# Kernel optimization log

Measured on AMD Instinct MI355X. Metric: run time of the kernel, lower is better.

## Reference

```python
import jax, jax.numpy as jnp
import numpy as np

MAX_ITER = 10
TAU = 1.0

def setup_inputs() -> dict:
    key = jax.random.key(0)
    s = jax.random.normal(key, (8192, 8192), dtype=jnp.float32)
    return {"s": s}

def reference(s) -> jnp.ndarray:
    # pygmtools sinkhorn (log-space): scale by 1/tau, then alternate
    # row-normalization (even iters) and column-normalization (odd iters)
    # via log-softmax; finally exponentiate.
    log_s = s / TAU
    for it in range(MAX_ITER):
        axis = 1 if it % 2 == 0 else 0  # rows first, then columns
        log_s = jax.nn.log_softmax(log_s, axis=axis)
    return jnp.exp(log_s)
```

## Files before the change

### kernel.cpp

```cpp
#include <hip/hip_runtime.h>
#include <math.h>

#define N 8192
#define NF4 2048


__device__ __forceinline__ float wave_max(float m) {
#pragma unroll
  for (int off = 32; off > 0; off >>= 1) m = fmaxf(m, __shfl_xor(m, off, 64));
  return m;
}
__device__ __forceinline__ float wave_sum(float s) {
#pragma unroll
  for (int off = 32; off > 0; off >>= 1) s += __shfl_xor(s, off, 64);
  return s;
}

__device__ __forceinline__ void process_row(
    const float4 (&buf)[8], const float4 (&vv)[8], float (&acc)[32],
    float* red, int parity, int wid, int lane, int t,
    float* __restrict__ u, int row) {
  float a[32];
#pragma unroll
  for (int k = 0; k < 8; ++k) {
    a[4 * k + 0] = buf[k].x - vv[k].x;
    a[4 * k + 1] = buf[k].y - vv[k].y;
    a[4 * k + 2] = buf[k].z - vv[k].z;
    a[4 * k + 3] = buf[k].w - vv[k].w;
  }
  float m0 = a[0], m1 = a[1], m2 = a[2], m3 = a[3];
#pragma unroll
  for (int k = 1; k < 8; ++k) {
    m0 = fmaxf(m0, a[4 * k + 0]);
    m1 = fmaxf(m1, a[4 * k + 1]);
    m2 = fmaxf(m2, a[4 * k + 2]);
    m3 = fmaxf(m3, a[4 * k + 3]);
  }
  float m = wave_max(fmaxf(fmaxf(m0, m1), fmaxf(m2, m3)));
  float* rp = red + (parity << 3);
  if (lane == 0) rp[wid] = m;
  __syncthreads();
  const float bm = fmaxf(fmaxf(rp[0], rp[1]), fmaxf(rp[2], rp[3]));
  float e[32];
  float s0 = 0.f, s1 = 0.f, s2 = 0.f, s3 = 0.f;
#pragma unroll
  for (int k = 0; k < 8; ++k) {
    e[4 * k + 0] = __expf(a[4 * k + 0] - bm);
    e[4 * k + 1] = __expf(a[4 * k + 1] - bm);
    e[4 * k + 2] = __expf(a[4 * k + 2] - bm);
    e[4 * k + 3] = __expf(a[4 * k + 3] - bm);
    s0 += e[4 * k + 0];
    s1 += e[4 * k + 1];
    s2 += e[4 * k + 2];
    s3 += e[4 * k + 3];
  }
  float ssum = wave_sum((s0 + s1) + (s2 + s3));
  if (lane == 0) rp[4 + wid] = ssum;
  __syncthreads();
  const float tot = rp[4] + rp[5] + rp[6] + rp[7];
  if (t == 0) u[row] = bm + __logf(tot);
  const float inv = 1.0f / tot;
#pragma unroll
  for (int i = 0; i < 32; ++i) acc[i] = fmaf(e[i], inv, acc[i]);
}

__global__ __launch_bounds__(256) void fused_pass(
    const float* __restrict__ s, const float* __restrict__ v,
    float* __restrict__ u, float* __restrict__ pt, int R, int use_v) {
  const int t = threadIdx.x;
  const int row0 = blockIdx.x * R;
  float4 vv[8];
  if (use_v) {
    const float4* v4 = (const float4*)v;
#pragma unroll
    for (int k = 0; k < 8; ++k) vv[k] = v4[t + k * 256];
  } else {
#pragma unroll
    for (int k = 0; k < 8; ++k) vv[k] = make_float4(0.f, 0.f, 0.f, 0.f);
  }
  float acc[32];
#pragma unroll
  for (int i = 0; i < 32; ++i) acc[i] = 0.f;
  __shared__ float red[16];
  const int wid = t >> 6, lane = t & 63;

  const float4* s4 = (const float4*)s + (size_t)row0 * NF4;
  float4 bufA[8], bufB[8];
#pragma unroll
  for (int k = 0; k < 8; ++k) bufA[k] = s4[t + k * 256];

  for (int r = 0; r < R; r += 2) {
    {
      const float4* p = s4 + (size_t)(r + 1) * NF4;
#pragma unroll
      for (int k = 0; k < 8; ++k) bufB[k] = p[t + k * 256];
    }
    process_row(bufA, vv, acc, red, 0, wid, lane, t, u, row0 + r);
    if (r + 2 < R) {
      const float4* p = s4 + (size_t)(r + 2) * NF4;
#pragma unroll
      for (int k = 0; k < 8; ++k) bufA[k] = p[t + k * 256];
    }
    process_row(bufB, vv, acc, red, 1, wid, lane, t, u, row0 + r + 1);
  }

  float4* p4 = (float4*)(pt + (size_t)blockIdx.x * N);
#pragma unroll
  for (int k = 0; k < 8; ++k)
    p4[t + k * 256] =
        make_float4(acc[4 * k], acc[4 * k + 1], acc[4 * k + 2], acc[4 * k + 3]);
}

__global__ __launch_bounds__(256) void combine1(const float* __restrict__ pt,
                                                float* __restrict__ ps,
                                                int per_group) {
  const int j = blockIdx.x * 256 + threadIdx.x;
  const int g = blockIdx.y;
  const float* p = pt + (size_t)g * per_group * N + j;
  float acc = 0.f;
  for (int c = 0; c < per_group; ++c) acc += p[(size_t)c * N];
  ps[(size_t)g * N + j] = acc;
}

__global__ __launch_bounds__(256) void combine2(const float* __restrict__ ps,
                                                float* __restrict__ v,
                                                int ngroups, int add_old) {
  const int j = blockIdx.x * 256 + threadIdx.x;
  float T = 0.f;
  for (int g = 0; g < ngroups; ++g) T += ps[(size_t)g * N + j];
  const float lv = __logf(T);
  v[j] = add_old ? v[j] + lv : lv;
}

__global__ __launch_bounds__(256) void finalize_k(const float* __restrict__ s,
                                                  const float* __restrict__ u,
                                                  const float* __restrict__ v,
                                                  float* __restrict__ out) {
  const size_t idx = (size_t)blockIdx.x * 256 + threadIdx.x;
  const int row = (int)(idx >> 11);
  const int c4 = (int)(idx & 2047);
  const float4 sv = ((const float4*)s)[idx];
  const float4 vv = ((const float4*)v)[c4];
  const float ur = u[row];
  float4 o;
  o.x = __expf(sv.x - ur - vv.x);
  o.y = __expf(sv.y - ur - vv.y);
  o.z = __expf(sv.z - ur - vv.z);
  o.w = __expf(sv.w - ur - vv.w);
  ((float4*)out)[idx] = o;
}

extern "C" void kernel_launch(void* const* d_in, const int* in_sizes, int n_in,
                              void* d_out, int out_size, void* d_ws, size_t ws_size,
                              hipStream_t stream) {
  const float* s = (const float*)d_in[0];
  float* out = (float*)d_out;
  float* ws = (float*)d_ws;

  const size_t avail = ws_size / sizeof(float);
  int nstrips = 512;
  while (nstrips > 8 && (size_t)(10 + nstrips) * N > avail) nstrips >>= 1;
  const int R = N / nstrips;
  float* u = ws;
  float* v = ws + N;
  float* ps = ws + 2 * N;
  float* pt = ws + 10 * N;
  const int G = (nstrips >= 8) ? 8 : nstrips;
  const int per_group = nstrips / G;

  for (int p = 0; p < 5; ++p) {
    fused_pass<<<nstrips, 256, 0, stream>>>(s, v, u, pt, R, p > 0 ? 1 : 0);
    combine1<<<dim3(N / 256, G), 256, 0, stream>>>(pt, ps, per_group);
    combine2<<<N / 256, 256, 0, stream>>>(ps, v, G, p > 0 ? 1 : 0);
  }
  finalize_k<<<(N / 256) * NF4, 256, 0, stream>>>(s, u, v, out);
}
```

Baseline: 782.2 us.

## Software-pipeline fused row pass across four register buffers with one barrier per row

Restructures the fused row-softmax pass into a staggered three-phase pipeline (max, exp/sum, accumulate) over four in-flight row buffers. Each row now costs one block barrier instead of two, and the loads for later rows are issued earlier to hide memory latency. The v offsets move from registers into shared memory to free registers for the extra buffers, with launch bounds asking for two blocks per CU. R becomes a template parameter, which lets the loops fully specialize. The risks are higher register pressure or spills from the four 8-float4 buffers, and extra LDS reads of v on every row.

```diff
diff --git a/kernel.cpp b/kernel.cpp
--- a/kernel.cpp
+++ b/kernel.cpp
@@ -16,93 +16,124 @@
   return s;
 }
 
-__device__ __forceinline__ void process_row(
-    const float4 (&buf)[8], const float4 (&vv)[8], float (&acc)[32],
-    float* red, int parity, int wid, int lane, int t,
-    float* __restrict__ u, int row) {
-  float a[32];
-#pragma unroll
-  for (int k = 0; k < 8; ++k) {
-    a[4 * k + 0] = buf[k].x - vv[k].x;
-    a[4 * k + 1] = buf[k].y - vv[k].y;
-    a[4 * k + 2] = buf[k].z - vv[k].z;
-    a[4 * k + 3] = buf[k].w - vv[k].w;
+template <int R>
+__global__ __launch_bounds__(256, 2) void fused_pass(
+    const float* __restrict__ s, const float* __restrict__ v,
+    float* __restrict__ u, float* __restrict__ pt, int use_v) {
+  static_assert(R % 4 == 0 && R >= 8, "pipeline needs R%4==0, R>=8");
+  const int t = threadIdx.x;
+  const int wid = t >> 6, lane = t & 63;
+  const int row0 = blockIdx.x * R;
+  __shared__ float4 vsh[8][256];
+  __shared__ float red[2][2][4];
+
+  {
+    const float4* v4 = (const float4*)v;
+#pragma unroll
+    for (int k = 0; k < 8; ++k)
+      vsh[k][t] = use_v ? v4[t + k * 256] : make_float4(0.f, 0.f, 0.f, 0.f);
   }
-  float m0 = a[0], m1 = a[1], m2 = a[2], m3 = a[3];
-#pragma unroll
-  for (int k = 1; k < 8; ++k) {
-    m0 = fmaxf(m0, a[4 * k + 0]);
-    m1 = fmaxf(m1, a[4 * k + 1]);
-    m2 = fmaxf(m2, a[4 * k + 2]);
-    m3 = fmaxf(m3, a[4 * k + 3]);
+
+  float acc[32];
+#pragma unroll
+  for (int i = 0; i < 32; ++i) acc[i] = 0.f;
+
+  const float4* s4 = (const float4*)s + (size_t)row0 * NF4;
+  float4 b0[8], b1[8], b2[8], b3[8];
+  float bmP = 0.f;
+
+  auto LOAD = [&](float4(&b)[8], int r) {
+    const float4* p = s4 + (size_t)r * NF4;
+#pragma unroll
+    for (int k = 0; k < 8; ++k) b[k] = p[t + k * 256];
+  };
+  auto P1 = [&](float4(&b)[8], int r) {
+    float m0 = -INFINITY, m1 = -INFINITY, m2 = -INFINITY, m3 = -INFINITY;
+#pragma unroll
+    for (int k = 0; k < 8; ++k) {
+      const float4 vv = vsh[k][t];
+      b[k].x -= vv.x; b[k].y -= vv.y; b[k].z -= vv.z; b[k].w -= vv.w;
+      m0 = fmaxf(m0, b[k].x); m1 = fmaxf(m1, b[k].y);
+      m2 = fmaxf(m2, b[k].z); m3 = fmaxf(m3, b[k].w);
+    }
+    const float m = wave_max(fmaxf(fmaxf(m0, m1), fmaxf(m2, m3)));
+    if (lane == 0) red[r & 1][0][wid] = m;
+  };
+  auto P2 = [&](float4(&b)[8], int r) -> float {
+    const float* rm = red[r & 1][0];
+    const float bm = fmaxf(fmaxf(rm[0], rm[1]), fmaxf(rm[2], rm[3]));
+    float s0 = 0.f, s1 = 0.f, s2 = 0.f, s3 = 0.f;
+#pragma unroll
+    for (int k = 0; k < 8; ++k) {
+      b[k].x = __expf(b[k].x - bm); b[k].y = __expf(b[k].y - bm);
+      b[k].z = __expf(b[k].z - bm); b[k].w = __expf(b[k].w - bm);
+      s0 += b[k].x; s1 += b[k].y; s2 += b[k].z; s3 += b[k].w;
+    }
+    const float ss = wave_sum((s0 + s1) + (s2 + s3));
+    if (lane == 0) red[r & 1][1][wid] = ss;
+    return bm;
+  };
+  auto P3 = [&](float4(&b)[8], int r, float bm) {
+    const float* rs = red[r & 1][1];
+    const float tot = (rs[0] + rs[1]) + (rs[2] + rs[3]);
+    const float inv = 1.0f / tot;
+#pragma unroll
+    for (int k = 0; k < 8; ++k) {
+      acc[4 * k + 0] = fmaf(b[k].x, inv, acc[4 * k + 0]);
+      acc[4 * k + 1] = fmaf(b[k].y, inv, acc[4 * k + 1]);
+      acc[4 * k + 2] = fmaf(b[k].z, inv, acc[4 * k + 2]);
+      acc[4 * k + 3] = fmaf(b[k].w, inv, acc[4 * k + 3]);
+    }
+    if (t == 0) u[row0 + r] = bm + __logf(tot);
+  };
+
+  LOAD(b0, 0);
+  LOAD(b1, 1);
+  P1(b0, 0);
+  __syncthreads();
+  LOAD(b2, 2);
+  bmP = P2(b0, 0);
+  P1(b1, 1);
+  __syncthreads();
+  LOAD(b3, 3);
+  P3(b0, 0, bmP);
+  bmP = P2(b1, 1);
+  P1(b2, 2);
+  __syncthreads();
+#pragma unroll 1
+  for (int k = 2; k <= R - 6; k += 4) {
+    LOAD(b0, k + 2);
+    P3(b1, k - 1, bmP);
+    bmP = P2(b2, k);
+    P1(b3, k + 1);
+    __syncthreads();
+
+    LOAD(b1, k + 3);
+    P3(b2, k, bmP);
+    bmP = P2(b3, k + 1);
+    P1(b0, k + 2);
+    __syncthreads();
+
+    LOAD(b2, k + 4);
+    P3(b3, k + 1, bmP);
+    bmP = P2(b0, k + 2);
+    P1(b1, k + 3);
+    __syncthreads();
+
+    LOAD(b3, k + 5);
+    P3(b0, k + 2, bmP);
+    bmP = P2(b1, k + 3);
+    P1(b2, k + 4);
+    __syncthreads();
   }
-  float m = wave_max(fmaxf(fmaxf(m0, m1), fmaxf(m2, m3)));
-  float* rp = red + (parity << 3);
-  if (lane == 0) rp[wid] = m;
-  __syncthreads();
-  const float bm = fmaxf(fmaxf(rp[0], rp[1]), fmaxf(rp[2], rp[3]));
-  float e[32];
-  float s0 = 0.f, s1 = 0.f, s2 = 0.f, s3 = 0.f;
-#pragma unroll
-  for (int k = 0; k < 8; ++k) {
-    e[4 * k + 0] = __expf(a[4 * k + 0] - bm);
-    e[4 * k + 1] = __expf(a[4 * k + 1] - bm);
-    e[4 * k + 2] = __expf(a[4 * k + 2] - bm);
-    e[4 * k + 3] = __expf(a[4 * k + 3] - bm);
-    s0 += e[4 * k + 0];
-    s1 += e[4 * k + 1];
-    s2 += e[4 * k + 2];
-    s3 += e[4 * k + 3];
-  }
-  float ssum = wave_sum((s0 + s1) + (s2 + s3));
-  if (lane == 0) rp[4 + wid] = ssum;
-  __syncthreads();
-  const float tot = rp[4] + rp[5] + rp[6] + rp[7];
-  if (t == 0) u[row] = bm + __logf(tot);
-  const float inv = 1.0f / tot;
-#pragma unroll
-  for (int i = 0; i < 32; ++i) acc[i] = fmaf(e[i], inv, acc[i]);
-}
-
-__global__ __launch_bounds__(256) void fused_pass(
-    const float* __restrict__ s, const float* __restrict__ v,
-    float* __restrict__ u, float* __restrict__ pt, int R, int use_v) {
-  const int t = threadIdx.x;
-  const int row0 = blockIdx.x * R;
-  float4 vv[8];
-  if (use_v) {
-    const float4* v4 = (const float4*)v;
-#pragma unroll
-    for (int k = 0; k < 8; ++k) vv[k] = v4[t + k * 256];
-  } else {
-#pragma unroll
-    for (int k = 0; k < 8; ++k) vv[k] = make_float4(0.f, 0.f, 0.f, 0.f);
-  }
-  float acc[32];
-#pragma unroll
-  for (int i = 0; i < 32; ++i) acc[i] = 0.f;
-  __shared__ float red[16];
-  const int wid = t >> 6, lane = t & 63;
-
-  const float4* s4 = (const float4*)s + (size_t)row0 * NF4;
-  float4 bufA[8], bufB[8];
-#pragma unroll
-  for (int k = 0; k < 8; ++k) bufA[k] = s4[t + k * 256];
-
-  for (int r = 0; r < R; r += 2) {
-    {
-      const float4* p = s4 + (size_t)(r + 1) * NF4;
-#pragma unroll
-      for (int k = 0; k < 8; ++k) bufB[k] = p[t + k * 256];
-    }
-    process_row(bufA, vv, acc, red, 0, wid, lane, t, u, row0 + r);
-    if (r + 2 < R) {
-      const float4* p = s4 + (size_t)(r + 2) * NF4;
-#pragma unroll
-      for (int k = 0; k < 8; ++k) bufA[k] = p[t + k * 256];
-    }
-    process_row(bufB, vv, acc, red, 1, wid, lane, t, u, row0 + r + 1);
-  }
+  P3(b1, R - 3, bmP);
+  bmP = P2(b2, R - 2);
+  P1(b3, R - 1);
+  __syncthreads();
+  P3(b2, R - 2, bmP);
+  bmP = P2(b3, R - 1);
+  __syncthreads();
+  P3(b3, R - 1, bmP);
 
   float4* p4 = (float4*)(pt + (size_t)blockIdx.x * N);
 #pragma unroll
@@ -159,17 +190,27 @@
 
   const size_t avail = ws_size / sizeof(float);
   int nstrips = 512;
-  while (nstrips > 8 && (size_t)(10 + nstrips) * N > avail) nstrips >>= 1;
-  const int R = N / nstrips;
+  while (nstrips > 128 && (size_t)(10 + nstrips) * N > avail) nstrips >>= 1;
   float* u = ws;
   float* v = ws + N;
   float* ps = ws + 2 * N;
   float* pt = ws + 10 * N;
-  const int G = (nstrips >= 8) ? 8 : nstrips;
+  const int G = 8;
   const int per_group = nstrips / G;
 
   for (int p = 0; p < 5; ++p) {
-    fused_pass<<<nstrips, 256, 0, stream>>>(s, v, u, pt, R, p > 0 ? 1 : 0);
+    const int use_v = p > 0 ? 1 : 0;
+    switch (nstrips) {
+      case 512:
+        fused_pass<16><<<512, 256, 0, stream>>>(s, v, u, pt, use_v);
+        break;
+      case 256:
+        fused_pass<32><<<256, 256, 0, stream>>>(s, v, u, pt, use_v);
+        break;
+      default:
+        fused_pass<64><<<128, 256, 0, stream>>>(s, v, u, pt, use_v);
+        break;
+    }
     combine1<<<dim3(N / 256, G), 256, 0, stream>>>(pt, ps, per_group);
     combine2<<<N / 256, 256, 0, stream>>>(ps, v, G, p > 0 ? 1 : 0);
   }
```

Result: slower. 964.2 us (+23.3%).

## Use 512-thread blocks with triple-buffered row prefetch and templated strip size

Applied to the files above, without the earlier changes.

The fused row pass now runs 512-thread blocks, so each thread holds 4 float4 per row instead of 8, which cuts register pressure and permits 4 blocks per CU. Row loads use a three-deep register ring buffer that prefetches two rows ahead, and the rows-per-strip count becomes a template parameter so the loop fully unrolls. The max/exp work is done in place in the load buffers to save registers. The trade-off is an eight-wave block reduction per row and a minimum strip count of 128.

```diff
diff --git a/kernel.cpp b/kernel.cpp
--- a/kernel.cpp
+++ b/kernel.cpp
@@ -16,99 +16,87 @@
   return s;
 }
 
-__device__ __forceinline__ void process_row(
-    const float4 (&buf)[8], const float4 (&vv)[8], float (&acc)[32],
-    float* red, int parity, int wid, int lane, int t,
-    float* __restrict__ u, int row) {
-  float a[32];
-#pragma unroll
-  for (int k = 0; k < 8; ++k) {
-    a[4 * k + 0] = buf[k].x - vv[k].x;
-    a[4 * k + 1] = buf[k].y - vv[k].y;
-    a[4 * k + 2] = buf[k].z - vv[k].z;
-    a[4 * k + 3] = buf[k].w - vv[k].w;
-  }
-  float m0 = a[0], m1 = a[1], m2 = a[2], m3 = a[3];
-#pragma unroll
-  for (int k = 1; k < 8; ++k) {
-    m0 = fmaxf(m0, a[4 * k + 0]);
-    m1 = fmaxf(m1, a[4 * k + 1]);
-    m2 = fmaxf(m2, a[4 * k + 2]);
-    m3 = fmaxf(m3, a[4 * k + 3]);
-  }
-  float m = wave_max(fmaxf(fmaxf(m0, m1), fmaxf(m2, m3)));
-  float* rp = red + (parity << 3);
-  if (lane == 0) rp[wid] = m;
-  __syncthreads();
-  const float bm = fmaxf(fmaxf(rp[0], rp[1]), fmaxf(rp[2], rp[3]));
-  float e[32];
-  float s0 = 0.f, s1 = 0.f, s2 = 0.f, s3 = 0.f;
-#pragma unroll
-  for (int k = 0; k < 8; ++k) {
-    e[4 * k + 0] = __expf(a[4 * k + 0] - bm);
-    e[4 * k + 1] = __expf(a[4 * k + 1] - bm);
-    e[4 * k + 2] = __expf(a[4 * k + 2] - bm);
-    e[4 * k + 3] = __expf(a[4 * k + 3] - bm);
-    s0 += e[4 * k + 0];
-    s1 += e[4 * k + 1];
-    s2 += e[4 * k + 2];
-    s3 += e[4 * k + 3];
-  }
-  float ssum = wave_sum((s0 + s1) + (s2 + s3));
-  if (lane == 0) rp[4 + wid] = ssum;
-  __syncthreads();
-  const float tot = rp[4] + rp[5] + rp[6] + rp[7];
-  if (t == 0) u[row] = bm + __logf(tot);
-  const float inv = 1.0f / tot;
-#pragma unroll
-  for (int i = 0; i < 32; ++i) acc[i] = fmaf(e[i], inv, acc[i]);
-}
+template <int R>
+__global__ __launch_bounds__(512, 4) void fused_pass(
+    const float* __restrict__ s, const float* __restrict__ v,
+    float* __restrict__ u, float* __restrict__ pt, int use_v) {
+  const int t = threadIdx.x;
+  const int wid = t >> 6, lane = t & 63;
+  const int row0 = blockIdx.x * R;
+  __shared__ float red[16];
 
-__global__ __launch_bounds__(256) void fused_pass(
-    const float* __restrict__ s, const float* __restrict__ v,
-    float* __restrict__ u, float* __restrict__ pt, int R, int use_v) {
-  const int t = threadIdx.x;
-  const int row0 = blockIdx.x * R;
-  float4 vv[8];
+  float4 vv[4];
   if (use_v) {
     const float4* v4 = (const float4*)v;
 #pragma unroll
-    for (int k = 0; k < 8; ++k) vv[k] = v4[t + k * 256];
+    for (int k = 0; k < 4; ++k) vv[k] = v4[t + k * 512];
   } else {
 #pragma unroll
-    for (int k = 0; k < 8; ++k) vv[k] = make_float4(0.f, 0.f, 0.f, 0.f);
+    for (int k = 0; k < 4; ++k) vv[k] = make_float4(0.f, 0.f, 0.f, 0.f);
   }
-  float acc[32];
+
+  float4 acc[4];
 #pragma unroll
-  for (int i = 0; i < 32; ++i) acc[i] = 0.f;
-  __shared__ float red[16];
-  const int wid = t >> 6, lane = t & 63;
+  for (int k = 0; k < 4; ++k) acc[k] = make_float4(0.f, 0.f, 0.f, 0.f);
 
   const float4* s4 = (const float4*)s + (size_t)row0 * NF4;
-  float4 bufA[8], bufB[8];
+  float4 bufs[3][4];
+
 #pragma unroll
-  for (int k = 0; k < 8; ++k) bufA[k] = s4[t + k * 256];
+  for (int k = 0; k < 4; ++k) bufs[0][k] = s4[t + k * 512];
+#pragma unroll
+  for (int k = 0; k < 4; ++k) bufs[1][k] = s4[NF4 + t + k * 512];
 
-  for (int r = 0; r < R; r += 2) {
-    {
-      const float4* p = s4 + (size_t)(r + 1) * NF4;
 #pragma unroll
-      for (int k = 0; k < 8; ++k) bufB[k] = p[t + k * 256];
-    }
-    process_row(bufA, vv, acc, red, 0, wid, lane, t, u, row0 + r);
+  for (int r = 0; r < R; ++r) {
+    float4(&cur)[4] = bufs[r % 3];
     if (r + 2 < R) {
       const float4* p = s4 + (size_t)(r + 2) * NF4;
+      float4(&nb)[4] = bufs[(r + 2) % 3];
 #pragma unroll
-      for (int k = 0; k < 8; ++k) bufA[k] = p[t + k * 256];
+      for (int k = 0; k < 4; ++k) nb[k] = p[t + k * 512];
     }
-    process_row(bufB, vv, acc, red, 1, wid, lane, t, u, row0 + r + 1);
+    float m0 = -INFINITY, m1 = -INFINITY, m2 = -INFINITY, m3 = -INFINITY;
+#pragma unroll
+    for (int k = 0; k < 4; ++k) {
+      cur[k].x -= vv[k].x; cur[k].y -= vv[k].y;
+      cur[k].z -= vv[k].z; cur[k].w -= vv[k].w;
+      m0 = fmaxf(m0, cur[k].x); m1 = fmaxf(m1, cur[k].y);
+      m2 = fmaxf(m2, cur[k].z); m3 = fmaxf(m3, cur[k].w);
+    }
+    const float m = wave_max(fmaxf(fmaxf(m0, m1), fmaxf(m2, m3)));
+    if (lane == 0) red[wid] = m;
+    __syncthreads();
+    float bm = red[0];
+#pragma unroll
+    for (int w = 1; w < 8; ++w) bm = fmaxf(bm, red[w]);
+    float s0 = 0.f, s1 = 0.f, s2 = 0.f, s3 = 0.f;
+#pragma unroll
+    for (int k = 0; k < 4; ++k) {
+      cur[k].x = __expf(cur[k].x - bm); cur[k].y = __expf(cur[k].y - bm);
+      cur[k].z = __expf(cur[k].z - bm); cur[k].w = __expf(cur[k].w - bm);
+      s0 += cur[k].x; s1 += cur[k].y; s2 += cur[k].z; s3 += cur[k].w;
+    }
+    const float ss = wave_sum((s0 + s1) + (s2 + s3));
+    if (lane == 0) red[8 + wid] = ss;
+    __syncthreads();
+    float tot = red[8];
+#pragma unroll
+    for (int w = 1; w < 8; ++w) tot += red[8 + w];
+    if (t == 0) u[row0 + r] = bm + __logf(tot);
+    const float inv = 1.0f / tot;
+#pragma unroll
+    for (int k = 0; k < 4; ++k) {
+      acc[k].x = fmaf(cur[k].x, inv, acc[k].x);
+      acc[k].y = fmaf(cur[k].y, inv, acc[k].y);
+      acc[k].z = fmaf(cur[k].z, inv, acc[k].z);
+      acc[k].w = fmaf(cur[k].w, inv, acc[k].w);
+    }
   }
 
   float4* p4 = (float4*)(pt + (size_t)blockIdx.x * N);
 #pragma unroll
-  for (int k = 0; k < 8; ++k)
-    p4[t + k * 256] =
-        make_float4(acc[4 * k], acc[4 * k + 1], acc[4 * k + 2], acc[4 * k + 3]);
+  for (int k = 0; k < 4; ++k) p4[t + k * 512] = acc[k];
 }
 
 __global__ __launch_bounds__(256) void combine1(const float* __restrict__ pt,
@@ -159,17 +147,27 @@
 
   const size_t avail = ws_size / sizeof(float);
   int nstrips = 512;
-  while (nstrips > 8 && (size_t)(10 + nstrips) * N > avail) nstrips >>= 1;
-  const int R = N / nstrips;
+  while (nstrips > 128 && (size_t)(10 + nstrips) * N > avail) nstrips >>= 1;
   float* u = ws;
   float* v = ws + N;
   float* ps = ws + 2 * N;
   float* pt = ws + 10 * N;
-  const int G = (nstrips >= 8) ? 8 : nstrips;
+  const int G = 8;
   const int per_group = nstrips / G;
 
   for (int p = 0; p < 5; ++p) {
-    fused_pass<<<nstrips, 256, 0, stream>>>(s, v, u, pt, R, p > 0 ? 1 : 0);
+    const int use_v = p > 0 ? 1 : 0;
+    switch (nstrips) {
+      case 512:
+        fused_pass<16><<<512, 512, 0, stream>>>(s, v, u, pt, use_v);
+        break;
+      case 256:
+        fused_pass<32><<<256, 512, 0, stream>>>(s, v, u, pt, use_v);
+        break;
+      default:
+        fused_pass<64><<<128, 512, 0, stream>>>(s, v, u, pt, use_v);
+        break;
+    }
     combine1<<<dim3(N / 256, G), 256, 0, stream>>>(pt, ps, per_group);
     combine2<<<N / 256, 256, 0, stream>>>(ps, v, G, p > 0 ? 1 : 0);
   }
```

Measured after the change: 1.234 ms. 57.7% more time.
